# Performance work log

Measured on AMD Instinct MI355X. Metric: run time of the kernel, lower is better.

The kernel has to match this reference:

```python
import jax, jax.numpy as jnp
import numpy as np

N_RAYS, N_SAMPLES = 8192, 128
RANK, RES = 32, 512


def setup_inputs() -> dict:
    key = jax.random.key(0)
    k0, k1, k2, k3 = jax.random.split(key, 4)
    pts = jax.random.uniform(k0, (N_RAYS, N_SAMPLES, 3), dtype=jnp.float32)
    # 3 plane grids for coord combos (0,1),(0,2),(1,2); torch shape [1,rank,H,W] -> [rank,H,W]
    grid_xy = jax.random.normal(k1, (RANK, RES, RES), dtype=jnp.float32) * 0.1
    grid_xz = jax.random.normal(k2, (RANK, RES, RES), dtype=jnp.float32) * 0.1
    grid_yz = jax.random.normal(k3, (RANK, RES, RES), dtype=jnp.float32) * 0.1
    aabb = jnp.array([[-1.0, -1.0, -1.0], [1.0, 1.0, 1.0]], dtype=jnp.float32)
    return {"pts": pts, "grid_xy": grid_xy, "grid_xz": grid_xz, "grid_yz": grid_yz, "aabb": aabb}


def _grid_sample2d(grid, coords):
    """Bilinear grid_sample, align_corners=True. grid [R,H,W], coords [N,2] in [-1,1] (x,y).
    Returns [N,R]."""
    H, W = grid.shape[1], grid.shape[2]
    x = (coords[:, 0] + 1.0) * 0.5 * (W - 1)
    y = (coords[:, 1] + 1.0) * 0.5 * (H - 1)
    x0 = jnp.floor(x)
    y0 = jnp.floor(y)
    wx = x - x0
    wy = y - y0
    x0i = jnp.clip(x0.astype(jnp.int32), 0, W - 1)
    x1i = jnp.clip(x0i + 1, 0, W - 1)
    y0i = jnp.clip(y0.astype(jnp.int32), 0, H - 1)
    y1i = jnp.clip(y0i + 1, 0, H - 1)
    v00 = grid[:, y0i, x0i]  # [R,N]
    v01 = grid[:, y0i, x1i]
    v10 = grid[:, y1i, x0i]
    v11 = grid[:, y1i, x1i]
    out = (v00 * (1 - wx) * (1 - wy) + v01 * wx * (1 - wy)
           + v10 * (1 - wx) * wy + v11 * wx * wy)
    return out.T  # [N,R]


def reference(pts, grid_xy, grid_xz, grid_yz, aabb):
    n_rays, n_samples, _ = pts.shape
    # normalize world coords to [-1,1]
    p = (pts - aabb[0]) * (2.0 / (aabb[1] - aabb[0])) - 1.0
    p = p.reshape(-1, 3)
    # multiply-reduce over the 3 coordinate-plane interpolations
    interp = (_grid_sample2d(grid_xy, p[:, (0, 1)])
              * _grid_sample2d(grid_xz, p[:, (0, 2)])
              * _grid_sample2d(grid_yz, p[:, (1, 2)]))  # [N, rank]
    density = jnp.mean(interp, axis=-1).reshape(n_rays, n_samples, 1)
    return jnp.exp(density)  # trunc_exp density activation
```

## Files before the change

### kernel.cpp

```cpp
#include <hip/hip_runtime.h>
#include <hip/hip_bf16.h>

#define RANK 32
#define RES  512

typedef __attribute__((ext_vector_type(2))) float f32x2;

__device__ __forceinline__ unsigned int pack4_fp8(float a, float b, float c, float d) {
    int v = 0;
    v = __builtin_amdgcn_cvt_pk_fp8_f32(a, b, v, false);
    v = __builtin_amdgcn_cvt_pk_fp8_f32(c, d, v, true);
    return (unsigned int)v;
}

struct AxisCoord { int i0; float w; };
__device__ __forceinline__ AxisCoord axis_coord(float c) {
    float x = (c + 1.0f) * 0.5f * (float)(RES - 1);
    float fx = floorf(x);
    AxisCoord a;
    a.w  = x - fx;
    int i = (int)fx;
    a.i0 = min(max(i, 0), RES - 1);
    return a;
}

struct PlaneCoord {
    int x0, y0;
    float w00, w01, w10, w11;
};

__device__ __forceinline__ PlaneCoord make_coord(float cx, float cy) {
    AxisCoord ax = axis_coord(cx);
    AxisCoord ay = axis_coord(cy);
    PlaneCoord c;
    c.x0 = ax.i0; c.y0 = ay.i0;
    float ix = 1.0f - ax.w, iy = 1.0f - ay.w;
    c.w00 = ix * iy; c.w01 = ax.w * iy; c.w10 = ix * ay.w; c.w11 = ax.w * ay.w;
    return c;
}

__global__ __launch_bounds__(256) void build_quads_kernel(
    const float* __restrict__ gxy, const float* __restrict__ gxz,
    const float* __restrict__ gyz, unsigned int* __restrict__ qout)
{
    __shared__ unsigned int lds[2][RES][RANK / 4];

    int bid   = blockIdx.x;
    int plane = bid >> 9;
    int y0    = bid & (RES - 1);
    const float* g = (plane == 0) ? gxy : ((plane == 1) ? gxz : gyz);
    int y1 = min(y0 + 1, RES - 1);
    int t  = threadIdx.x;
    int xa = t * 2;

    #pragma unroll
    for (int row = 0; row < 2; ++row) {
        int yy = row ? y1 : y0;
        const float* gr = g + (size_t)yy * RES + xa;
        #pragma unroll
        for (int rq = 0; rq < RANK / 4; ++rq) {
            f32x2 f0 = *reinterpret_cast<const f32x2*>(gr + (size_t)(rq * 4 + 0) * RES * RES);
            f32x2 f1 = *reinterpret_cast<const f32x2*>(gr + (size_t)(rq * 4 + 1) * RES * RES);
            f32x2 f2 = *reinterpret_cast<const f32x2*>(gr + (size_t)(rq * 4 + 2) * RES * RES);
            f32x2 f3 = *reinterpret_cast<const f32x2*>(gr + (size_t)(rq * 4 + 3) * RES * RES);
            lds[row][xa    ][rq] = pack4_fp8(f0.x, f1.x, f2.x, f3.x);
            lds[row][xa + 1][rq] = pack4_fp8(f0.y, f1.y, f2.y, f3.y);
        }
    }
    __syncthreads();

    #pragma unroll
    for (int k = 0; k < 2; ++k) {
        int xr = t + k * 256;
        int x1 = min(xr + 1, RES - 1);
        uint4* dst = reinterpret_cast<uint4*>(qout) +
                     ((size_t)plane * RES * RES + (size_t)y0 * RES + xr) * 8;
        const unsigned int* t00 = lds[0][xr];
        const unsigned int* t01 = lds[0][x1];
        const unsigned int* t10 = lds[1][xr];
        const unsigned int* t11 = lds[1][x1];
        uint4 u;
        u.x = t00[0]; u.y = t00[1]; u.z = t00[2]; u.w = t00[3]; dst[0] = u;
        u.x = t00[4]; u.y = t00[5]; u.z = t00[6]; u.w = t00[7]; dst[1] = u;
        u.x = t01[0]; u.y = t01[1]; u.z = t01[2]; u.w = t01[3]; dst[2] = u;
        u.x = t01[4]; u.y = t01[5]; u.z = t01[6]; u.w = t01[7]; dst[3] = u;
        u.x = t10[0]; u.y = t10[1]; u.z = t10[2]; u.w = t10[3]; dst[4] = u;
        u.x = t10[4]; u.y = t10[5]; u.z = t10[6]; u.w = t10[7]; dst[5] = u;
        u.x = t11[0]; u.y = t11[1]; u.z = t11[2]; u.w = t11[3]; dst[6] = u;
        u.x = t11[4]; u.y = t11[5]; u.z = t11[6]; u.w = t11[7]; dst[7] = u;
    }
}

__device__ __forceinline__ void decode_quad(const uint4* __restrict__ stage,
                                            int c, int lane,
                                            float w00, float w01, float w10, float w11,
                                            f32x2* __restrict__ v)
{
    const float wt[4] = { w00, w01, w10, w11 };
    #pragma unroll
    for (int jj = 0; jj < 8; ++jj) {
        uint4 q = stage[(c * 64 + lane) * 8 + (jj ^ (lane & 7))];
        float wk = wt[jj >> 1];
        int vb = (jj & 1) * 8;
        unsigned int w_[4] = { q.x, q.y, q.z, q.w };
        #pragma unroll
        for (int d = 0; d < 4; ++d) {
            f32x2 lo = __builtin_amdgcn_cvt_pk_f32_fp8((int)w_[d], false);
            f32x2 hi = __builtin_amdgcn_cvt_pk_f32_fp8((int)w_[d], true);
            int k0 = vb + d * 2, k1 = k0 + 1;
            if (jj < 2) {
                v[k0].x = wk * lo.x; v[k0].y = wk * lo.y;
                v[k1].x = wk * hi.x; v[k1].y = wk * hi.y;
            } else {
                v[k0].x = fmaf(wk, lo.x, v[k0].x);
                v[k0].y = fmaf(wk, lo.y, v[k0].y);
                v[k1].x = fmaf(wk, hi.x, v[k1].x);
                v[k1].y = fmaf(wk, hi.y, v[k1].y);
            }
        }
    }
}

__device__ __forceinline__ void decode_quad_reg(const uint4 q[8],
                                                float w00, float w01, float w10, float w11,
                                                f32x2* __restrict__ v)
{
    const float wt[4] = { w00, w01, w10, w11 };
    #pragma unroll
    for (int jj = 0; jj < 8; ++jj) {
        float wk = wt[jj >> 1];
        int vb = (jj & 1) * 8;
        unsigned int w_[4] = { q[jj].x, q[jj].y, q[jj].z, q[jj].w };
        #pragma unroll
        for (int d = 0; d < 4; ++d) {
            f32x2 lo = __builtin_amdgcn_cvt_pk_f32_fp8((int)w_[d], false);
            f32x2 hi = __builtin_amdgcn_cvt_pk_f32_fp8((int)w_[d], true);
            int k0 = vb + d * 2, k1 = k0 + 1;
            if (jj < 2) {
                v[k0].x = wk * lo.x; v[k0].y = wk * lo.y;
                v[k1].x = wk * hi.x; v[k1].y = wk * hi.y;
            } else {
                v[k0].x = fmaf(wk, lo.x, v[k0].x);
                v[k0].y = fmaf(wk, lo.y, v[k0].y);
                v[k1].x = fmaf(wk, hi.x, v[k1].x);
                v[k1].y = fmaf(wk, hi.y, v[k1].y);
            }
        }
    }
}

__global__ __launch_bounds__(64) void sample_quad_kernel(
    const float* __restrict__ pts, const unsigned char* __restrict__ table,
    const float* __restrict__ aabb, float* __restrict__ out)
{
    __shared__ __align__(16) uint4 stage[3 * 64 * 8];

    int lane = threadIdx.x;
    int idx  = blockIdx.x * 64 + lane;

    float px = pts[idx * 3 + 0];
    float py = pts[idx * 3 + 1];
    float pz = pts[idx * 3 + 2];

    float lox = aabb[0], loy = aabb[1], loz = aabb[2];
    float hix = aabb[3], hiy = aabb[4], hiz = aabb[5];

    float pnx = (px - lox) * (2.0f / (hix - lox)) - 1.0f;
    float pny = (py - loy) * (2.0f / (hiy - loy)) - 1.0f;
    float pnz = (pz - loz) * (2.0f / (hiz - loz)) - 1.0f;

    PlaneCoord cxy = make_coord(pnx, pny);
    PlaneCoord cxz = make_coord(pnx, pnz);
    PlaneCoord cyz = make_coord(pny, pnz);

    int offs[3];
    offs[0] = ((0 * RES + cxy.y0) * RES + cxy.x0) * 128;
    offs[1] = ((1 * RES + cxz.y0) * RES + cxz.x0) * 128;
    offs[2] = ((2 * RES + cyz.y0) * RES + cyz.x0) * 128;

    int p_sub = lane >> 3;
    int sw    = (lane & 7) ^ p_sub;

#if __has_builtin(__builtin_amdgcn_global_load_lds)
    #pragma unroll
    for (int i = 0; i < 24; ++i) {
        const int c = i >> 3;
        const int b = i & 7;
        int p = b * 8 + p_sub;
        unsigned int off = (unsigned int)__shfl(offs[c], p);
        const unsigned char* gp = table + off + sw * 16;
        unsigned int* lp = (unsigned int*)&stage[(c * 64 + b * 8) * 8];
        __builtin_amdgcn_global_load_lds(
            (const __attribute__((address_space(1))) unsigned int*)gp,
            (__attribute__((address_space(3))) unsigned int*)lp, 16, 0, 0);
        if ((i & 7) == 7) __builtin_amdgcn_sched_barrier(0);
    }

    f32x2 pa[16], pb[16];
    asm volatile("s_waitcnt vmcnt(16)" ::: "memory");
    decode_quad(stage, 0, lane, cxy.w00, cxy.w01, cxy.w10, cxy.w11, pa);
    asm volatile("s_waitcnt vmcnt(8)" ::: "memory");
    decode_quad(stage, 1, lane, cxz.w00, cxz.w01, cxz.w10, cxz.w11, pb);
    #pragma unroll
    for (int k = 0; k < 16; ++k) { pa[k].x *= pb[k].x; pa[k].y *= pb[k].y; }
    asm volatile("s_waitcnt vmcnt(0)" ::: "memory");
    decode_quad(stage, 2, lane, cyz.w00, cyz.w01, cyz.w10, cyz.w11, pb);
#else
    uint4 qa[8], qb[8], qc[8];
    #pragma unroll
    for (int i = 0; i < 8; ++i) qa[i] = *reinterpret_cast<const uint4*>(table + offs[0] + i * 16);
    #pragma unroll
    for (int i = 0; i < 8; ++i) qb[i] = *reinterpret_cast<const uint4*>(table + offs[1] + i * 16);
    #pragma unroll
    for (int i = 0; i < 8; ++i) qc[i] = *reinterpret_cast<const uint4*>(table + offs[2] + i * 16);
    f32x2 pa[16], pb[16];
    decode_quad_reg(qa, cxy.w00, cxy.w01, cxy.w10, cxy.w11, pa);
    decode_quad_reg(qb, cxz.w00, cxz.w01, cxz.w10, cxz.w11, pb);
    #pragma unroll
    for (int k = 0; k < 16; ++k) { pa[k].x *= pb[k].x; pa[k].y *= pb[k].y; }
    decode_quad_reg(qc, cyz.w00, cyz.w01, cyz.w10, cyz.w11, pb);
#endif

    float sx = 0.0f, sy = 0.0f;
    #pragma unroll
    for (int k = 0; k < 16; ++k) {
        sx = fmaf(pa[k].x, pb[k].x, sx);
        sy = fmaf(pa[k].y, pb[k].y, sy);
    }
    out[idx] = expf((sx + sy) * (1.0f / (float)RANK));
}

__global__ __launch_bounds__(256) void sample_direct_kernel(
    const float* __restrict__ pts,
    const float* __restrict__ gxy, const float* __restrict__ gxz,
    const float* __restrict__ gyz,
    const float* __restrict__ aabb, float* __restrict__ out, int npts)
{
    int idx = blockIdx.x * 256 + threadIdx.x;
    if (idx >= npts) return;

    float px = pts[idx * 3 + 0];
    float py = pts[idx * 3 + 1];
    float pz = pts[idx * 3 + 2];

    float lox = aabb[0], loy = aabb[1], loz = aabb[2];
    float hix = aabb[3], hiy = aabb[4], hiz = aabb[5];

    float pnx = (px - lox) * (2.0f / (hix - lox)) - 1.0f;
    float pny = (py - loy) * (2.0f / (hiy - loy)) - 1.0f;
    float pnz = (pz - loz) * (2.0f / (hiz - loz)) - 1.0f;

    AxisCoord ax = axis_coord(pnx);
    AxisCoord ay = axis_coord(pny);
    AxisCoord az = axis_coord(pnz);
    int ax1 = min(ax.i0 + 1, RES - 1);
    int ay1 = min(ay.i0 + 1, RES - 1);
    int az1 = min(az.i0 + 1, RES - 1);

    float axw = ax.w, ayw = ay.w, azw = az.w;

    int o_xy00 = ay.i0 * RES + ax.i0, o_xy01 = ay.i0 * RES + ax1;
    int o_xy10 = ay1  * RES + ax.i0, o_xy11 = ay1  * RES + ax1;
    int o_xz00 = az.i0 * RES + ax.i0, o_xz01 = az.i0 * RES + ax1;
    int o_xz10 = az1  * RES + ax.i0, o_xz11 = az1  * RES + ax1;
    int o_yz00 = az.i0 * RES + ay.i0, o_yz01 = az.i0 * RES + ay1;
    int o_yz10 = az1  * RES + ay.i0, o_yz11 = az1  * RES + ay1;

    float sum = 0.0f;
    for (int r = 0; r < RANK; ++r) {
        size_t pbs = (size_t)r * RES * RES;
        float vxy = (1-axw)*(1-ayw)*gxy[pbs+o_xy00] + axw*(1-ayw)*gxy[pbs+o_xy01]
                  + (1-axw)*ayw   *gxy[pbs+o_xy10] + axw*ayw   *gxy[pbs+o_xy11];
        float vxz = (1-axw)*(1-azw)*gxz[pbs+o_xz00] + axw*(1-azw)*gxz[pbs+o_xz01]
                  + (1-axw)*azw   *gxz[pbs+o_xz10] + axw*azw   *gxz[pbs+o_xz11];
        float vyz = (1-ayw)*(1-azw)*gyz[pbs+o_yz00] + ayw*(1-azw)*gyz[pbs+o_yz01]
                  + (1-ayw)*azw   *gyz[pbs+o_yz10] + ayw*azw   *gyz[pbs+o_yz11];
        sum += vxy * vxz * vyz;
    }
    out[idx] = expf(sum * (1.0f / (float)RANK));
}

extern "C" void kernel_launch(void* const* d_in, const int* in_sizes, int n_in,
                              void* d_out, int out_size, void* d_ws, size_t ws_size,
                              hipStream_t stream) {
    const float* pts  = (const float*)d_in[0];
    const float* gxy  = (const float*)d_in[1];
    const float* gxz  = (const float*)d_in[2];
    const float* gyz  = (const float*)d_in[3];
    const float* aabb = (const float*)d_in[4];
    float* out = (float*)d_out;

    int npts = in_sizes[0] / 3;

    size_t need_quad = (size_t)3 * RES * RES * 128;

    if (ws_size >= need_quad && (npts % 64) == 0) {
        unsigned int* tbl = (unsigned int*)d_ws;
        build_quads_kernel<<<3 * RES, 256, 0, stream>>>(gxy, gxz, gyz, tbl);
        sample_quad_kernel<<<npts / 64, 64, 0, stream>>>(
            pts, (const unsigned char*)tbl, aabb, out);
    } else {
        int nblk = (npts + 255) / 256;
        sample_direct_kernel<<<nblk, 256, 0, stream>>>(pts, gxy, gxz, gyz, aabb, out, npts);
    }
}
```

Before: 230.5 us.

## Shrink LDS staging to two buffers and vectorize fp8 decode math

Cuts the per-block LDS stage from three plane buffers to two. The third plane's gather is issued into the first buffer once that buffer has been copied into registers, which lowers LDS use per 64-thread block and should allow more blocks per CU. Decode now runs from registers using packed f32x2 multiply and fma, and the precompute kernel writes the table with nontemporal stores. The final exp uses the fast __expf intrinsic, which trades a little accuracy for speed.

```diff
diff --git a/kernel.cpp b/kernel.cpp
--- a/kernel.cpp
+++ b/kernel.cpp
@@ -5,6 +5,9 @@
 #define RES  512
 
 typedef __attribute__((ext_vector_type(2))) float f32x2;
+typedef __attribute__((ext_vector_type(4))) unsigned int u32x4;
+
+__device__ __forceinline__ f32x2 make2(float w) { f32x2 r; r.x = w; r.y = w; return r; }
 
 __device__ __forceinline__ unsigned int pack4_fp8(float a, float b, float c, float d) {
     int v = 0;
@@ -73,62 +76,32 @@
     for (int k = 0; k < 2; ++k) {
         int xr = t + k * 256;
         int x1 = min(xr + 1, RES - 1);
-        uint4* dst = reinterpret_cast<uint4*>(qout) +
+        u32x4* dst = reinterpret_cast<u32x4*>(qout) +
                      ((size_t)plane * RES * RES + (size_t)y0 * RES + xr) * 8;
         const unsigned int* t00 = lds[0][xr];
         const unsigned int* t01 = lds[0][x1];
         const unsigned int* t10 = lds[1][xr];
         const unsigned int* t11 = lds[1][x1];
-        uint4 u;
-        u.x = t00[0]; u.y = t00[1]; u.z = t00[2]; u.w = t00[3]; dst[0] = u;
-        u.x = t00[4]; u.y = t00[5]; u.z = t00[6]; u.w = t00[7]; dst[1] = u;
-        u.x = t01[0]; u.y = t01[1]; u.z = t01[2]; u.w = t01[3]; dst[2] = u;
-        u.x = t01[4]; u.y = t01[5]; u.z = t01[6]; u.w = t01[7]; dst[3] = u;
-        u.x = t10[0]; u.y = t10[1]; u.z = t10[2]; u.w = t10[3]; dst[4] = u;
-        u.x = t10[4]; u.y = t10[5]; u.z = t10[6]; u.w = t10[7]; dst[5] = u;
-        u.x = t11[0]; u.y = t11[1]; u.z = t11[2]; u.w = t11[3]; dst[6] = u;
-        u.x = t11[4]; u.y = t11[5]; u.z = t11[6]; u.w = t11[7]; dst[7] = u;
-    }
-}
-
-__device__ __forceinline__ void decode_quad(const uint4* __restrict__ stage,
-                                            int c, int lane,
-                                            float w00, float w01, float w10, float w11,
-                                            f32x2* __restrict__ v)
-{
-    const float wt[4] = { w00, w01, w10, w11 };
-    #pragma unroll
-    for (int jj = 0; jj < 8; ++jj) {
-        uint4 q = stage[(c * 64 + lane) * 8 + (jj ^ (lane & 7))];
-        float wk = wt[jj >> 1];
-        int vb = (jj & 1) * 8;
-        unsigned int w_[4] = { q.x, q.y, q.z, q.w };
-        #pragma unroll
-        for (int d = 0; d < 4; ++d) {
-            f32x2 lo = __builtin_amdgcn_cvt_pk_f32_fp8((int)w_[d], false);
-            f32x2 hi = __builtin_amdgcn_cvt_pk_f32_fp8((int)w_[d], true);
-            int k0 = vb + d * 2, k1 = k0 + 1;
-            if (jj < 2) {
-                v[k0].x = wk * lo.x; v[k0].y = wk * lo.y;
-                v[k1].x = wk * hi.x; v[k1].y = wk * hi.y;
-            } else {
-                v[k0].x = fmaf(wk, lo.x, v[k0].x);
-                v[k0].y = fmaf(wk, lo.y, v[k0].y);
-                v[k1].x = fmaf(wk, hi.x, v[k1].x);
-                v[k1].y = fmaf(wk, hi.y, v[k1].y);
-            }
-        }
-    }
-}
-
-__device__ __forceinline__ void decode_quad_reg(const uint4 q[8],
+        u32x4 u;
+        u.x = t00[0]; u.y = t00[1]; u.z = t00[2]; u.w = t00[3]; __builtin_nontemporal_store(u, dst + 0);
+        u.x = t00[4]; u.y = t00[5]; u.z = t00[6]; u.w = t00[7]; __builtin_nontemporal_store(u, dst + 1);
+        u.x = t01[0]; u.y = t01[1]; u.z = t01[2]; u.w = t01[3]; __builtin_nontemporal_store(u, dst + 2);
+        u.x = t01[4]; u.y = t01[5]; u.z = t01[6]; u.w = t01[7]; __builtin_nontemporal_store(u, dst + 3);
+        u.x = t10[0]; u.y = t10[1]; u.z = t10[2]; u.w = t10[3]; __builtin_nontemporal_store(u, dst + 4);
+        u.x = t10[4]; u.y = t10[5]; u.z = t10[6]; u.w = t10[7]; __builtin_nontemporal_store(u, dst + 5);
+        u.x = t11[0]; u.y = t11[1]; u.z = t11[2]; u.w = t11[3]; __builtin_nontemporal_store(u, dst + 6);
+        u.x = t11[4]; u.y = t11[5]; u.z = t11[6]; u.w = t11[7]; __builtin_nontemporal_store(u, dst + 7);
+    }
+}
+
+__device__ __forceinline__ void decode_quad_reg(const u32x4 q[8],
                                                 float w00, float w01, float w10, float w11,
                                                 f32x2* __restrict__ v)
 {
     const float wt[4] = { w00, w01, w10, w11 };
     #pragma unroll
     for (int jj = 0; jj < 8; ++jj) {
-        float wk = wt[jj >> 1];
+        f32x2 wk = make2(wt[jj >> 1]);
         int vb = (jj & 1) * 8;
         unsigned int w_[4] = { q[jj].x, q[jj].y, q[jj].z, q[jj].w };
         #pragma unroll
@@ -137,13 +110,11 @@
             f32x2 hi = __builtin_amdgcn_cvt_pk_f32_fp8((int)w_[d], true);
             int k0 = vb + d * 2, k1 = k0 + 1;
             if (jj < 2) {
-                v[k0].x = wk * lo.x; v[k0].y = wk * lo.y;
-                v[k1].x = wk * hi.x; v[k1].y = wk * hi.y;
+                v[k0] = lo * wk;
+                v[k1] = hi * wk;
             } else {
-                v[k0].x = fmaf(wk, lo.x, v[k0].x);
-                v[k0].y = fmaf(wk, lo.y, v[k0].y);
-                v[k1].x = fmaf(wk, hi.x, v[k1].x);
-                v[k1].y = fmaf(wk, hi.y, v[k1].y);
+                v[k0] = __builtin_elementwise_fma(lo, wk, v[k0]);
+                v[k1] = __builtin_elementwise_fma(hi, wk, v[k1]);
             }
         }
     }
@@ -153,7 +124,7 @@
     const float* __restrict__ pts, const unsigned char* __restrict__ table,
     const float* __restrict__ aabb, float* __restrict__ out)
 {
-    __shared__ __align__(16) uint4 stage[3 * 64 * 8];
+    __shared__ __align__(16) u32x4 stage[2][64][8];
 
     int lane = threadIdx.x;
     int idx  = blockIdx.x * 64 + lane;
@@ -183,42 +154,67 @@
 
 #if __has_builtin(__builtin_amdgcn_global_load_lds)
     #pragma unroll
-    for (int i = 0; i < 24; ++i) {
+    for (int i = 0; i < 16; ++i) {
         const int c = i >> 3;
         const int b = i & 7;
         int p = b * 8 + p_sub;
         unsigned int off = (unsigned int)__shfl(offs[c], p);
         const unsigned char* gp = table + off + sw * 16;
-        unsigned int* lp = (unsigned int*)&stage[(c * 64 + b * 8) * 8];
+        unsigned int* lp = (unsigned int*)&stage[c][b * 8][0];
         __builtin_amdgcn_global_load_lds(
             (const __attribute__((address_space(1))) unsigned int*)gp,
             (__attribute__((address_space(3))) unsigned int*)lp, 16, 0, 0);
-        if ((i & 7) == 7) __builtin_amdgcn_sched_barrier(0);
-    }
+    }
+    __builtin_amdgcn_sched_barrier(0);
 
     f32x2 pa[16], pb[16];
-    asm volatile("s_waitcnt vmcnt(16)" ::: "memory");
-    decode_quad(stage, 0, lane, cxy.w00, cxy.w01, cxy.w10, cxy.w11, pa);
+    u32x4 q[8];
+
     asm volatile("s_waitcnt vmcnt(8)" ::: "memory");
-    decode_quad(stage, 1, lane, cxz.w00, cxz.w01, cxz.w10, cxz.w11, pb);
-    #pragma unroll
-    for (int k = 0; k < 16; ++k) { pa[k].x *= pb[k].x; pa[k].y *= pb[k].y; }
+    #pragma unroll
+    for (int jj = 0; jj < 8; ++jj) q[jj] = stage[0][lane][jj ^ (lane & 7)];
+    asm volatile("s_waitcnt lgkmcnt(0)" ::: "memory");
+    __builtin_amdgcn_sched_barrier(0);
+
+    #pragma unroll
+    for (int b = 0; b < 8; ++b) {
+        int p = b * 8 + p_sub;
+        unsigned int off = (unsigned int)__shfl(offs[2], p);
+        const unsigned char* gp = table + off + sw * 16;
+        unsigned int* lp = (unsigned int*)&stage[0][b * 8][0];
+        __builtin_amdgcn_global_load_lds(
+            (const __attribute__((address_space(1))) unsigned int*)gp,
+            (__attribute__((address_space(3))) unsigned int*)lp, 16, 0, 0);
+    }
+    __builtin_amdgcn_sched_barrier(0);
+
+    decode_quad_reg(q, cxy.w00, cxy.w01, cxy.w10, cxy.w11, pa);
+
+    asm volatile("s_waitcnt vmcnt(8)" ::: "memory");
+    #pragma unroll
+    for (int jj = 0; jj < 8; ++jj) q[jj] = stage[1][lane][jj ^ (lane & 7)];
+    decode_quad_reg(q, cxz.w00, cxz.w01, cxz.w10, cxz.w11, pb);
+    #pragma unroll
+    for (int k = 0; k < 16; ++k) pa[k] *= pb[k];
+
     asm volatile("s_waitcnt vmcnt(0)" ::: "memory");
-    decode_quad(stage, 2, lane, cyz.w00, cyz.w01, cyz.w10, cyz.w11, pb);
+    #pragma unroll
+    for (int jj = 0; jj < 8; ++jj) q[jj] = stage[0][lane][jj ^ (lane & 7)];
+    decode_quad_reg(q, cyz.w00, cyz.w01, cyz.w10, cyz.w11, pb);
 #else
-    uint4 qa[8], qb[8], qc[8];
-    #pragma unroll
-    for (int i = 0; i < 8; ++i) qa[i] = *reinterpret_cast<const uint4*>(table + offs[0] + i * 16);
-    #pragma unroll
-    for (int i = 0; i < 8; ++i) qb[i] = *reinterpret_cast<const uint4*>(table + offs[1] + i * 16);
-    #pragma unroll
-    for (int i = 0; i < 8; ++i) qc[i] = *reinterpret_cast<const uint4*>(table + offs[2] + i * 16);
     f32x2 pa[16], pb[16];
-    decode_quad_reg(qa, cxy.w00, cxy.w01, cxy.w10, cxy.w11, pa);
-    decode_quad_reg(qb, cxz.w00, cxz.w01, cxz.w10, cxz.w11, pb);
-    #pragma unroll
-    for (int k = 0; k < 16; ++k) { pa[k].x *= pb[k].x; pa[k].y *= pb[k].y; }
-    decode_quad_reg(qc, cyz.w00, cyz.w01, cyz.w10, cyz.w11, pb);
+    u32x4 q[8];
+    #pragma unroll
+    for (int i = 0; i < 8; ++i) q[i] = *reinterpret_cast<const u32x4*>(table + offs[0] + i * 16);
+    decode_quad_reg(q, cxy.w00, cxy.w01, cxy.w10, cxy.w11, pa);
+    #pragma unroll
+    for (int i = 0; i < 8; ++i) q[i] = *reinterpret_cast<const u32x4*>(table + offs[1] + i * 16);
+    decode_quad_reg(q, cxz.w00, cxz.w01, cxz.w10, cxz.w11, pb);
+    #pragma unroll
+    for (int k = 0; k < 16; ++k) pa[k] *= pb[k];
+    #pragma unroll
+    for (int i = 0; i < 8; ++i) q[i] = *reinterpret_cast<const u32x4*>(table + offs[2] + i * 16);
+    decode_quad_reg(q, cyz.w00, cyz.w01, cyz.w10, cyz.w11, pb);
 #endif
 
     float sx = 0.0f, sy = 0.0f;
@@ -227,7 +223,7 @@
         sx = fmaf(pa[k].x, pb[k].x, sx);
         sy = fmaf(pa[k].y, pb[k].y, sy);
     }
-    out[idx] = expf((sx + sy) * (1.0f / (float)RANK));
+    out[idx] = __expf((sx + sy) * (1.0f / (float)RANK));
 }
 
 __global__ __launch_bounds__(256) void sample_direct_kernel(
```

Measured after the change: 428.8 us. +86.0%, slower.
